# Kernel optimization log

Hardware: AMD Instinct MI355X
Metric: run time of the kernel (lower is better)

The kernel has to match this reference:

```python
import jax, jax.numpy as jnp
import numpy as np

CHANNELS = 1024
PIVOT = 16384


def setup_inputs() -> dict:
    key = jax.random.key(0)
    k1, k2, k3 = jax.random.split(key, 3)
    x_Jx = jax.random.normal(k1, (3 * PIVOT, CHANNELS), dtype=jnp.float32)
    # Linear(channels, channels) params, torch-like init scale
    s = 1.0 / np.sqrt(CHANNELS)
    W = jax.random.uniform(k2, (CHANNELS, CHANNELS), dtype=jnp.float32, minval=-s, maxval=s)
    b = jax.random.uniform(k3, (CHANNELS,), dtype=jnp.float32, minval=-s, maxval=s)
    return {"x_Jx": x_Jx, "W": W, "b": b}


def reference(x_Jx, W, b):
    pivot = x_Jx.shape[0] // 3
    channels = W.shape[0]
    x = x_Jx[:pivot]                                   # [P, C]
    hAx = jnp.tanh(x @ W.T + b)                        # [P, C]
    hpAx = 1.0 - hAx ** 2                              # tanh'
    Jx = x_Jx[pivot:].reshape(pivot, channels, 2)      # [P, C, 2]
    # sum_j W[i,j] * Jx[p,j,k]  (the explicit broadcast-sum in torch is this GEMM)
    WJx = jnp.einsum('ij,pjk->pik', W, Jx)             # [P, C, 2]
    hpAJx = (hpAx[:, :, None] * WJx).reshape(-1, channels)  # [2P, C]
    return jnp.concatenate([hAx, hpAJx], axis=0)       # [3P, C]
```

## Files before the change

### kernel.cpp

```cpp
#include <hip/hip_runtime.h>
#include <hip/hip_bf16.h>
#include <cstdint>

typedef __attribute__((ext_vector_type(8))) short short8;
typedef __attribute__((ext_vector_type(4))) float floatx4;

__device__ __forceinline__ float tanh_fast(float x) {
    float e = __expf(2.0f * x);
    return 1.0f - 2.0f * __builtin_amdgcn_rcpf(e + 1.0f);
}

__device__ __forceinline__ unsigned int bf16_bits(float f) {
    __hip_bfloat16 h = __float2bfloat16(f);
    return (unsigned int)*reinterpret_cast<unsigned short*>(&h);
}
__device__ __forceinline__ unsigned int pack2(float lo, float hi) {
    return bf16_bits(lo) | (bf16_bits(hi) << 16);
}

__device__ __forceinline__ void async16(const void* g, void* l) {
    __builtin_amdgcn_global_load_lds(
        (const __attribute__((address_space(1))) unsigned int*)g,
        (__attribute__((address_space(3))) unsigned int*)l, 16, 0, 0);
}

__device__ __forceinline__ void swizzle_tile(int& row0, int& col0) {
    const int nwg  = gridDim.x * gridDim.y;
    const int flat = blockIdx.y * gridDim.x + blockIdx.x;
    const int swz  = (flat & 7) * (nwg >> 3) + (flat >> 3);
    col0 = (swz & 7) * 128;
    row0 = (swz >> 3) * 128;
}


__global__ __launch_bounds__(256) void cvt_prep(
    const float* __restrict__ X, const float* __restrict__ G,
    const float* __restrict__ W,
    short* __restrict__ Xb, short* __restrict__ Mb, short* __restrict__ Wb,
    int nbX, int nbG)
{
    const int tid = threadIdx.x;
    const int b   = blockIdx.x;
    if (b < nbX) {
        const size_t e = ((size_t)b * 256 + tid) * 16;
        const float4 f0 = *(const float4*)(X + e);
        const float4 f1 = *(const float4*)(X + e + 4);
        const float4 f2 = *(const float4*)(X + e + 8);
        const float4 f3 = *(const float4*)(X + e + 12);
        uint4 o0, o1;
        o0.x = pack2(f0.x, f0.y); o0.y = pack2(f0.z, f0.w);
        o0.z = pack2(f1.x, f1.y); o0.w = pack2(f1.z, f1.w);
        o1.x = pack2(f2.x, f2.y); o1.y = pack2(f2.z, f2.w);
        o1.z = pack2(f3.x, f3.y); o1.w = pack2(f3.z, f3.w);
        *(uint4*)(Xb + e)     = o0;
        *(uint4*)(Xb + e + 8) = o1;
    } else if (b < nbX + nbG) {
        const size_t s = (size_t)(b - nbX) * 256 + tid;
        const size_t p = s >> 7;
        const int    c = (int)(s & 127);
        const float* src = G + p * 2048 + (size_t)c * 16;
        const float4 f0 = *(const float4*)(src);
        const float4 f1 = *(const float4*)(src + 4);
        const float4 f2 = *(const float4*)(src + 8);
        const float4 f3 = *(const float4*)(src + 12);
        uint4 E, O;
        E.x = pack2(f0.x, f0.z); E.y = pack2(f1.x, f1.z);
        E.z = pack2(f2.x, f2.z); E.w = pack2(f3.x, f3.z);
        O.x = pack2(f0.y, f0.w); O.y = pack2(f1.y, f1.w);
        O.z = pack2(f2.y, f2.w); O.w = pack2(f3.y, f3.w);
        *(uint4*)(Mb + (2 * p)     * 1024 + (size_t)c * 8) = E;
        *(uint4*)(Mb + (2 * p + 1) * 1024 + (size_t)c * 8) = O;
    } else {
        const size_t e = ((size_t)(b - nbX - nbG) * 256 + tid) * 16;
        const float4 f0 = *(const float4*)(W + e);
        const float4 f1 = *(const float4*)(W + e + 4);
        const float4 f2 = *(const float4*)(W + e + 8);
        const float4 f3 = *(const float4*)(W + e + 12);
        uint4 o0, o1;
        o0.x = pack2(f0.x, f0.y); o0.y = pack2(f0.z, f0.w);
        o0.z = pack2(f1.x, f1.y); o0.w = pack2(f1.z, f1.w);
        o1.x = pack2(f2.x, f2.y); o1.y = pack2(f2.z, f2.w);
        o1.z = pack2(f3.x, f3.y); o1.w = pack2(f3.z, f3.w);
        *(uint4*)(Wb + e)     = o0;
        *(uint4*)(Wb + e + 8) = o1;
    }
}

#define GEMM_STAGE_AND_MMA(Ag, Bg)                                             \
    for (int k0 = 0; k0 < K; k0 += 64) {                                       \
        __syncthreads();                                                       \
        _Pragma("unroll")                                                      \
        for (int i = 0; i < 4; ++i) {                                          \
            async16(Ag + (size_t)i * 8 * K + k0, Al + i * 512);                \
            async16(Bg + (size_t)i * 8 * K + k0, Bl + i * 512);                \
        }                                                                      \
        __syncthreads();                                                       \
        _Pragma("unroll")                                                      \
        for (int ki = 0; ki < 2; ++ki) {                                       \
            const int kxs = (((ki * 4 + quad) ^ rxor)) * 8;                    \
            short8 af[4], bf[4];                                               \
            _Pragma("unroll")                                                  \
            for (int s = 0; s < 4; ++s)                                        \
                af[s] = *(const short8*)&As[a_base + s * 16 * 64 + kxs];       \
            _Pragma("unroll")                                                  \
            for (int s = 0; s < 4; ++s)                                        \
                bf[s] = *(const short8*)&Bs[b_base + s * 16 * 64 + kxs];       \
            _Pragma("unroll")                                                  \
            for (int a = 0; a < 4; ++a)                                        \
                _Pragma("unroll")                                              \
                for (int b = 0; b < 4; ++b)                                    \
                    acc[a][b] = __builtin_amdgcn_mfma_f32_16x16x32_bf16(       \
                        af[a], bf[b], acc[a][b], 0, 0, 0);                     \
        }                                                                      \
    }

__global__ __launch_bounds__(256) void k1b_gemm_tanh(
    const short* __restrict__ A,
    const short* __restrict__ B,
    const float* __restrict__ Bv,
    float* __restrict__ out, int K)
{
    __shared__ __align__(16) short As[128 * 64];
    __shared__ __align__(16) short Bs[128 * 64];

    const int tid  = threadIdx.x;
    const int lane = tid & 63;
    const int wave = tid >> 6;
    const int wm = wave & 1, wn = wave >> 1;

    int row0, col0;
    swizzle_tile(row0, col0);

    const int l15  = lane & 15;
    const int quad = lane >> 4;
    const int rxor = l15 & 7;
    const int a_base = (wm * 64 + l15) * 64;
    const int b_base = (wn * 64 + l15) * 64;

    const int lrow = lane >> 3;
    const int lcol = lane & 7;
    const int cswz = lcol ^ lrow;
    const short* Ag = A + (size_t)(row0 + wave * 32 + lrow) * K + cswz * 8;
    const short* Bg = B + (size_t)(col0 + wave * 32 + lrow) * K + cswz * 8;
    short* Al = As + wave * 32 * 64;
    short* Bl = Bs + wave * 32 * 64;

    floatx4 acc[4][4];
#pragma unroll
    for (int a = 0; a < 4; ++a)
#pragma unroll
        for (int b = 0; b < 4; ++b) acc[a][b] = (floatx4){0.f, 0.f, 0.f, 0.f};

    GEMM_STAGE_AND_MMA(Ag, Bg)

    float bv[4];
#pragma unroll
    for (int b = 0; b < 4; ++b)
        bv[b] = Bv[col0 + wn * 64 + b * 16 + l15];

#pragma unroll
    for (int a = 0; a < 4; ++a) {
        const int rbase = row0 + wm * 64 + a * 16 + quad * 4;
#pragma unroll
        for (int b = 0; b < 4; ++b) {
            const int n = col0 + wn * 64 + b * 16 + l15;
#pragma unroll
            for (int r = 0; r < 4; ++r)
                out[(size_t)(rbase + r) * 1024 + n] = tanh_fast(acc[a][b][r] + bv[b]);
        }
    }
}

__global__ __launch_bounds__(256) void k2b_gemm_jac(
    const short* __restrict__ A,
    const short* __restrict__ B,
    const float* __restrict__ Hout,
    float* __restrict__ out2, int K)
{
    __shared__ __align__(16) short As[128 * 64];
    __shared__ __align__(16) short Bs[128 * 64];

    const int tid  = threadIdx.x;
    const int lane = tid & 63;
    const int wave = tid >> 6;
    const int wm = wave & 1, wn = wave >> 1;

    int r0, col0;
    swizzle_tile(r0, col0);

    const int l15  = lane & 15;
    const int quad = lane >> 4;
    const int rxor = l15 & 7;
    const int a_base = (wm * 64 + l15) * 64;
    const int b_base = (wn * 64 + l15) * 64;

    const int lrow = lane >> 3;
    const int lcol = lane & 7;
    const int cswz = lcol ^ lrow;
    const short* Ag = A + (size_t)(r0 + wave * 32 + lrow) * K + cswz * 8;
    const short* Bg = B + (size_t)(col0 + wave * 32 + lrow) * K + cswz * 8;
    short* Al = As + wave * 32 * 64;
    short* Bl = Bs + wave * 32 * 64;

    floatx4 acc[4][4];
#pragma unroll
    for (int a = 0; a < 4; ++a)
#pragma unroll
        for (int b = 0; b < 4; ++b) acc[a][b] = (floatx4){0.f, 0.f, 0.f, 0.f};

    GEMM_STAGE_AND_MMA(Ag, Bg)

#pragma unroll
    for (int a = 0; a < 4; ++a) {
        const int rb = r0 + wm * 64 + a * 16 + quad * 4;
#pragma unroll
        for (int b = 0; b < 4; ++b) {
            const int i = col0 + wn * 64 + b * 16 + l15;
            const int shift = (i >= 512) ? 1 : 0;
            const int ccol = 2 * i - shift * 1024;
#pragma unroll
            for (int pr = 0; pr < 2; ++pr) {
                const int re = rb + pr * 2;
                const int p  = re >> 1;
                const float h  = Hout[(size_t)p * 1024 + i];
                const float hp = 1.0f - h * h;
                float2 st;
                st.x = hp * acc[a][b][pr * 2];
                st.y = hp * acc[a][b][pr * 2 + 1];
                *(float2*)&out2[(size_t)(re + shift) * 1024 + ccol] = st;
            }
        }
    }
}

#define LDS_STRIDE 72

__global__ __launch_bounds__(256) void k1_gemm_tanh(
    const float* __restrict__ X, const float* __restrict__ W,
    const float* __restrict__ Bv, float* __restrict__ out, int K)
{
    __shared__ __align__(16) short As[128 * LDS_STRIDE];
    __shared__ __align__(16) short Bs[128 * LDS_STRIDE];
    const int tid  = threadIdx.x;
    const int lane = tid & 63;
    const int wave = tid >> 6;
    const int wm = wave & 1, wn = wave >> 1;
    int row0, col0;
    swizzle_tile(row0, col0);
    const int l15  = lane & 15;
    const int quad = lane >> 4;
    const int a_base = (wm * 64 + l15) * LDS_STRIDE;
    const int b_base = (wn * 64 + l15) * LDS_STRIDE;

    floatx4 acc[4][4];
#pragma unroll
    for (int a = 0; a < 4; ++a)
#pragma unroll
        for (int b = 0; b < 4; ++b) acc[a][b] = (floatx4){0.f, 0.f, 0.f, 0.f};

    for (int k0 = 0; k0 < K; k0 += 64) {
        __syncthreads();
#pragma unroll
        for (int i = 0; i < 8; ++i) {
            const int g = i * 256 + tid;
            const int r = g >> 4, c = g & 15;
            const float4 va = *(const float4*)(X + (size_t)(row0 + r) * K + k0 + c * 4);
            const float4 vb = *(const float4*)(W + (size_t)(col0 + r) * K + k0 + c * 4);
            uint2 ea, eb;
            ea.x = pack2(va.x, va.y); ea.y = pack2(va.z, va.w);
            eb.x = pack2(vb.x, vb.y); eb.y = pack2(vb.z, vb.w);
            *(uint2*)&As[r * LDS_STRIDE + c * 4] = ea;
            *(uint2*)&Bs[r * LDS_STRIDE + c * 4] = eb;
        }
        __syncthreads();
#pragma unroll
        for (int ki = 0; ki < 2; ++ki) {
            const int kx = ki * 32 + quad * 8;
            short8 af[4], bf[4];
#pragma unroll
            for (int s = 0; s < 4; ++s)
                af[s] = *(const short8*)&As[a_base + s * 16 * LDS_STRIDE + kx];
#pragma unroll
            for (int s = 0; s < 4; ++s)
                bf[s] = *(const short8*)&Bs[b_base + s * 16 * LDS_STRIDE + kx];
#pragma unroll
            for (int a = 0; a < 4; ++a)
#pragma unroll
                for (int b = 0; b < 4; ++b)
                    acc[a][b] = __builtin_amdgcn_mfma_f32_16x16x32_bf16(
                        af[a], bf[b], acc[a][b], 0, 0, 0);
        }
    }

    float bv[4];
#pragma unroll
    for (int b = 0; b < 4; ++b)
        bv[b] = Bv[col0 + wn * 64 + b * 16 + l15];
#pragma unroll
    for (int a = 0; a < 4; ++a) {
        const int rbase = row0 + wm * 64 + a * 16 + quad * 4;
#pragma unroll
        for (int b = 0; b < 4; ++b) {
            const int n = col0 + wn * 64 + b * 16 + l15;
#pragma unroll
            for (int r = 0; r < 4; ++r)
                out[(size_t)(rbase + r) * 1024 + n] = tanh_fast(acc[a][b][r] + bv[b]);
        }
    }
}

__global__ __launch_bounds__(256) void k2_gemm_jac(
    const float* __restrict__ G, const float* __restrict__ W,
    const float* __restrict__ Hout, float* __restrict__ out2, int K)
{
    __shared__ __align__(16) short As[128 * LDS_STRIDE];
    __shared__ __align__(16) short Bs[128 * LDS_STRIDE];
    const int tid  = threadIdx.x;
    const int lane = tid & 63;
    const int wave = tid >> 6;
    const int wm = wave & 1, wn = wave >> 1;
    int r0, col0;
    swizzle_tile(r0, col0);
    const int p0 = r0 >> 1;
    const int l15  = lane & 15;
    const int quad = lane >> 4;
    const int a_base = (wm * 64 + l15) * LDS_STRIDE;
    const int b_base = (wn * 64 + l15) * LDS_STRIDE;

    floatx4 acc[4][4];
#pragma unroll
    for (int a = 0; a < 4; ++a)
#pragma unroll
        for (int b = 0; b < 4; ++b) acc[a][b] = (floatx4){0.f, 0.f, 0.f, 0.f};

    for (int k0 = 0; k0 < K; k0 += 64) {
        __syncthreads();
#pragma unroll
        for (int i = 0; i < 8; ++i) {
            const int g = i * 256 + tid;
            const int r = g >> 4, c = g & 15;
            const float4 vb = *(const float4*)(W + (size_t)(col0 + r) * K + k0 + c * 4);
            uint2 eb;
            eb.x = pack2(vb.x, vb.y); eb.y = pack2(vb.z, vb.w);
            *(uint2*)&Bs[r * LDS_STRIDE + c * 4] = eb;
        }
#pragma unroll
        for (int i = 0; i < 4; ++i) {
            const int g = i * 256 + tid;
            const int q = g >> 4, d = g & 15;
            const float* src = G + (size_t)(p0 + q) * 2048 + 2 * k0 + d * 8;
            const float4 u0 = *(const float4*)src;
            const float4 u1 = *(const float4*)(src + 4);
            uint2 E, O;
            E.x = pack2(u0.x, u0.z); E.y = pack2(u1.x, u1.z);
            O.x = pack2(u0.y, u0.w); O.y = pack2(u1.y, u1.w);
            *(uint2*)&As[(2 * q)     * LDS_STRIDE + d * 4] = E;
            *(uint2*)&As[(2 * q + 1) * LDS_STRIDE + d * 4] = O;
        }
        __syncthreads();
#pragma unroll
        for (int ki = 0; ki < 2; ++ki) {
            const int kx = ki * 32 + quad * 8;
            short8 af[4], bf[4];
#pragma unroll
            for (int s = 0; s < 4; ++s)
                af[s] = *(const short8*)&As[a_base + s * 16 * LDS_STRIDE + kx];
#pragma unroll
            for (int s = 0; s < 4; ++s)
                bf[s] = *(const short8*)&Bs[b_base + s * 16 * LDS_STRIDE + kx];
#pragma unroll
            for (int a = 0; a < 4; ++a)
#pragma unroll
                for (int b = 0; b < 4; ++b)
                    acc[a][b] = __builtin_amdgcn_mfma_f32_16x16x32_bf16(
                        af[a], bf[b], acc[a][b], 0, 0, 0);
        }
    }

#pragma unroll
    for (int a = 0; a < 4; ++a) {
        const int rb = r0 + wm * 64 + a * 16 + quad * 4;
#pragma unroll
        for (int b = 0; b < 4; ++b) {
            const int i = col0 + wn * 64 + b * 16 + l15;
            const int shift = (i >= 512) ? 1 : 0;
            const int ccol = 2 * i - shift * 1024;
#pragma unroll
            for (int pr = 0; pr < 2; ++pr) {
                const int re = rb + pr * 2;
                const int p  = re >> 1;
                const float h  = Hout[(size_t)p * 1024 + i];
                const float hp = 1.0f - h * h;
                float2 st;
                st.x = hp * acc[a][b][pr * 2];
                st.y = hp * acc[a][b][pr * 2 + 1];
                *(float2*)&out2[(size_t)(re + shift) * 1024 + ccol] = st;
            }
        }
    }
}

extern "C" void kernel_launch(void* const* d_in, const int* in_sizes, int n_in,
                              void* d_out, int out_size, void* d_ws, size_t ws_size,
                              hipStream_t stream) {
    const float* xJx = (const float*)d_in[0];
    const float* W   = (const float*)d_in[1];
    const float* bv  = (const float*)d_in[2];
    float* out = (float*)d_out;

    const int C     = 1024;
    const int rows3 = in_sizes[0] / C;
    const int pivot = rows3 / 3;

    const size_t szXb = (size_t)pivot * C * 2;
    const size_t szMb = (size_t)2 * pivot * C * 2;
    const size_t szWb = (size_t)C * C * 2;
    dim3 blk(256);

    if (ws_size >= szXb + szMb + szWb) {
        short* Xb = (short*)d_ws;
        short* Mb = (short*)((char*)d_ws + szXb);
        short* Wb = (short*)((char*)d_ws + szXb + szMb);

        const int nbX = (pivot * C) / 4096;
        const int nbG = (pivot * 2 * C) / 4096;
        const int nbW = (C * C) / 4096;
        cvt_prep<<<dim3(nbX + nbG + nbW), blk, 0, stream>>>(
            xJx, xJx + (size_t)pivot * C, W, Xb, Mb, Wb, nbX, nbG);

        dim3 g1(C / 128, pivot / 128);
        k1b_gemm_tanh<<<g1, blk, 0, stream>>>(Xb, Wb, bv, out, C);

        dim3 g2(C / 128, (2 * pivot) / 128);
        k2b_gemm_jac<<<g2, blk, 0, stream>>>(Mb, Wb, out,
                                             out + (size_t)pivot * C, C);
    } else {
        dim3 g1(C / 128, pivot / 128);
        k1_gemm_tanh<<<g1, blk, 0, stream>>>(xJx, W, bv, out, C);
        dim3 g2(C / 128, (2 * pivot) / 128);
        k2_gemm_jac<<<g2, blk, 0, stream>>>(xJx + (size_t)pivot * C, W, out,
                                            out + (size_t)pivot * C, C);
    }
}
```

Measured before the change: 508.5 us.

## Double-buffer LDS tiles to overlap global loads with MFMA compute

Both GEMM kernels (tanh and Jacobian) now use two LDS buffers per operand. The next K-tile's async global-to-LDS loads are issued before the MFMAs on the current tile, which also cuts the loop to one barrier per iteration instead of two. The goal is to hide global memory latency behind matrix math. In exchange LDS per block doubles to 64KB, which can lower the number of resident blocks per CU.

```diff
diff --git a/kernel.cpp b/kernel.cpp
--- a/kernel.cpp
+++ b/kernel.cpp
@@ -86,31 +86,48 @@
     }
 }
 
-#define GEMM_STAGE_AND_MMA(Ag, Bg)                                             \
-    for (int k0 = 0; k0 < K; k0 += 64) {                                       \
-        __syncthreads();                                                       \
+#define GEMM_PIPELINED(Ag, Bg)                                                 \
+    {                                                                          \
+        const int nt = K >> 6;                                                 \
         _Pragma("unroll")                                                      \
         for (int i = 0; i < 4; ++i) {                                          \
-            async16(Ag + (size_t)i * 8 * K + k0, Al + i * 512);                \
-            async16(Bg + (size_t)i * 8 * K + k0, Bl + i * 512);                \
+            async16(Ag + (size_t)i * 8 * K, As + wave * 2048 + i * 512);       \
+            async16(Bg + (size_t)i * 8 * K, Bs + wave * 2048 + i * 512);       \
         }                                                                      \
         __syncthreads();                                                       \
-        _Pragma("unroll")                                                      \
-        for (int ki = 0; ki < 2; ++ki) {                                       \
-            const int kxs = (((ki * 4 + quad) ^ rxor)) * 8;                    \
-            short8 af[4], bf[4];                                               \
+        for (int t = 0; t < nt; ++t) {                                         \
+            const short* Asc = As + (t & 1) * 8192;                            \
+            const short* Bsc = Bs + (t & 1) * 8192;                            \
+            if (t + 1 < nt) {                                                  \
+                short* Asn = As + ((t + 1) & 1) * 8192;                        \
+                short* Bsn = Bs + ((t + 1) & 1) * 8192;                        \
+                const int kn = (t + 1) * 64;                                   \
+                _Pragma("unroll")                                              \
+                for (int i = 0; i < 4; ++i) {                                  \
+                    async16(Ag + (size_t)i * 8 * K + kn,                       \
+                            Asn + wave * 2048 + i * 512);                      \
+                    async16(Bg + (size_t)i * 8 * K + kn,                       \
+                            Bsn + wave * 2048 + i * 512);                      \
+                }                                                              \
+            }                                                                  \
             _Pragma("unroll")                                                  \
-            for (int s = 0; s < 4; ++s)                                        \
-                af[s] = *(const short8*)&As[a_base + s * 16 * 64 + kxs];       \
-            _Pragma("unroll")                                                  \
-            for (int s = 0; s < 4; ++s)                                        \
-                bf[s] = *(const short8*)&Bs[b_base + s * 16 * 64 + kxs];       \
-            _Pragma("unroll")                                                  \
-            for (int a = 0; a < 4; ++a)                                        \
+            for (int ki = 0; ki < 2; ++ki) {                                   \
+                const int kxs = ((ki * 4 + quad) ^ rxor) * 8;                  \
+                short8 af[4], bf[4];                                           \
                 _Pragma("unroll")                                              \
-                for (int b = 0; b < 4; ++b)                                    \
-                    acc[a][b] = __builtin_amdgcn_mfma_f32_16x16x32_bf16(       \
-                        af[a], bf[b], acc[a][b], 0, 0, 0);                     \
+                for (int s = 0; s < 4; ++s)                                    \
+                    af[s] = *(const short8*)&Asc[a_base + s * 1024 + kxs];     \
+                _Pragma("unroll")                                              \
+                for (int s = 0; s < 4; ++s)                                    \
+                    bf[s] = *(const short8*)&Bsc[b_base + s * 1024 + kxs];     \
+                _Pragma("unroll")                                              \
+                for (int a = 0; a < 4; ++a)                                    \
+                    _Pragma("unroll")                                          \
+                    for (int b = 0; b < 4; ++b)                                \
+                        acc[a][b] = __builtin_amdgcn_mfma_f32_16x16x32_bf16(   \
+                            af[a], bf[b], acc[a][b], 0, 0, 0);                 \
+            }                                                                  \
+            __syncthreads();                                                   \
         }                                                                      \
     }
 
@@ -120,8 +137,8 @@
     const float* __restrict__ Bv,
     float* __restrict__ out, int K)
 {
-    __shared__ __align__(16) short As[128 * 64];
-    __shared__ __align__(16) short Bs[128 * 64];
+    __shared__ __align__(16) short As[2 * 128 * 64];
+    __shared__ __align__(16) short Bs[2 * 128 * 64];
 
     const int tid  = threadIdx.x;
     const int lane = tid & 63;
@@ -142,8 +159,6 @@
     const int cswz = lcol ^ lrow;
     const short* Ag = A + (size_t)(row0 + wave * 32 + lrow) * K + cswz * 8;
     const short* Bg = B + (size_t)(col0 + wave * 32 + lrow) * K + cswz * 8;
-    short* Al = As + wave * 32 * 64;
-    short* Bl = Bs + wave * 32 * 64;
 
     floatx4 acc[4][4];
 #pragma unroll
@@ -151,7 +166,7 @@
 #pragma unroll
         for (int b = 0; b < 4; ++b) acc[a][b] = (floatx4){0.f, 0.f, 0.f, 0.f};
 
-    GEMM_STAGE_AND_MMA(Ag, Bg)
+    GEMM_PIPELINED(Ag, Bg)
 
     float bv[4];
 #pragma unroll
@@ -177,8 +192,8 @@
     const float* __restrict__ Hout,
     float* __restrict__ out2, int K)
 {
-    __shared__ __align__(16) short As[128 * 64];
-    __shared__ __align__(16) short Bs[128 * 64];
+    __shared__ __align__(16) short As[2 * 128 * 64];
+    __shared__ __align__(16) short Bs[2 * 128 * 64];
 
     const int tid  = threadIdx.x;
     const int lane = tid & 63;
@@ -199,8 +214,6 @@
     const int cswz = lcol ^ lrow;
     const short* Ag = A + (size_t)(r0 + wave * 32 + lrow) * K + cswz * 8;
     const short* Bg = B + (size_t)(col0 + wave * 32 + lrow) * K + cswz * 8;
-    short* Al = As + wave * 32 * 64;
-    short* Bl = Bs + wave * 32 * 64;
 
     floatx4 acc[4][4];
 #pragma unroll
@@ -208,7 +221,7 @@
 #pragma unroll
         for (int b = 0; b < 4; ++b) acc[a][b] = (floatx4){0.f, 0.f, 0.f, 0.f};
 
-    GEMM_STAGE_AND_MMA(Ag, Bg)
+    GEMM_PIPELINED(Ag, Bg)
 
 #pragma unroll
     for (int a = 0; a < 4; ++a) {
```

Result: no change. 503.5 us (-1.0%).

## Use 256x256 tiles with 8 waves and double-buffered LDS prefetch in bf16 GEMMs

Applied to the files above, without the earlier changes.

The bf16 GEMM kernels move from 128x128 tiles with 4 waves to 256x256 tiles with 8 waves, each wave computing a 128x64 block. The LDS is double-buffered so the next K-slice loads asynchronously while the current one is being multiplied, with one barrier per iteration. MFMA sections are bracketed with s_setprio. The goal is more operand reuse per byte loaded and overlap of global loads with compute. In exchange it uses 128 KB of LDS and 128 accumulator registers per lane, leaving one block per CU, and halves the number of workgroups.

```diff
diff --git a/kernel.cpp b/kernel.cpp
--- a/kernel.cpp
+++ b/kernel.cpp
@@ -24,12 +24,13 @@
         (__attribute__((address_space(3))) unsigned int*)l, 16, 0, 0);
 }
 
-__device__ __forceinline__ void swizzle_tile(int& row0, int& col0) {
-    const int nwg  = gridDim.x * gridDim.y;
-    const int flat = blockIdx.y * gridDim.x + blockIdx.x;
+__device__ __forceinline__ void swizzle_tile_bm(int& row0, int& col0, int bm) {
+    const int gx   = gridDim.x;
+    const int nwg  = gx * gridDim.y;
+    const int flat = blockIdx.y * gx + blockIdx.x;
     const int swz  = (flat & 7) * (nwg >> 3) + (flat >> 3);
-    col0 = (swz & 7) * 128;
-    row0 = (swz >> 3) * 128;
+    col0 = (swz % gx) * bm;
+    row0 = (swz / gx) * bm;
 }
 
 
@@ -86,136 +87,162 @@
     }
 }
 
-#define GEMM_STAGE_AND_MMA(Ag, Bg)                                             \
-    for (int k0 = 0; k0 < K; k0 += 64) {                                       \
-        __syncthreads();                                                       \
+#define STAGE256(dst_d, kt)                                                    \
+    {                                                                          \
+        const int koff = (kt) * 64;                                            \
         _Pragma("unroll")                                                      \
         for (int i = 0; i < 4; ++i) {                                          \
-            async16(Ag + (size_t)i * 8 * K + k0, Al + i * 512);                \
-            async16(Bg + (size_t)i * 8 * K + k0, Bl + i * 512);                \
+            async16(Ag + (size_t)(i * 64) * K + koff,                          \
+                    As + (dst_d) * 16384 + (i * 64 + wave * 8) * 64);          \
+            async16(Bg + (size_t)(i * 64) * K + koff,                          \
+                    Bs + (dst_d) * 16384 + (i * 64 + wave * 8) * 64);          \
         }                                                                      \
-        __syncthreads();                                                       \
-        _Pragma("unroll")                                                      \
-        for (int ki = 0; ki < 2; ++ki) {                                       \
-            const int kxs = (((ki * 4 + quad) ^ rxor)) * 8;                    \
-            short8 af[4], bf[4];                                               \
+    }
+
+#define GEMM256_MAIN()                                                         \
+    {                                                                          \
+        const int NT = K >> 6;                                                 \
+        STAGE256(0, 0)                                                         \
+        asm volatile("s_waitcnt vmcnt(0)" ::: "memory");                       \
+        __builtin_amdgcn_s_barrier();                                          \
+        for (int t = 0; t < NT; ++t) {                                         \
+            const int d = t & 1;                                               \
+            if (t + 1 < NT) STAGE256(d ^ 1, t + 1)                             \
+            const short* Ad = As + d * 16384;                                  \
+            const short* Bd = Bs + d * 16384;                                  \
+            short8 bfr[4][2];                                                  \
             _Pragma("unroll")                                                  \
-            for (int s = 0; s < 4; ++s)                                        \
-                af[s] = *(const short8*)&As[a_base + s * 16 * 64 + kxs];       \
+            for (int n = 0; n < 4; ++n)                                        \
+                _Pragma("unroll")                                              \
+                for (int ki = 0; ki < 2; ++ki)                                 \
+                    bfr[n][ki] = *(const short8*)&Bd[b_base + n * 1024 +       \
+                                     (((ki * 4 + quad) ^ rxor) * 8)];          \
             _Pragma("unroll")                                                  \
-            for (int s = 0; s < 4; ++s)                                        \
-                bf[s] = *(const short8*)&Bs[b_base + s * 16 * 64 + kxs];       \
-            _Pragma("unroll")                                                  \
-            for (int a = 0; a < 4; ++a)                                        \
+            for (int p = 0; p < 4; ++p) {                                      \
+                short8 afr[2][2];                                              \
                 _Pragma("unroll")                                              \
-                for (int b = 0; b < 4; ++b)                                    \
-                    acc[a][b] = __builtin_amdgcn_mfma_f32_16x16x32_bf16(       \
-                        af[a], bf[b], acc[a][b], 0, 0, 0);                     \
+                for (int a2 = 0; a2 < 2; ++a2)                                 \
+                    _Pragma("unroll")                                          \
+                    for (int ki = 0; ki < 2; ++ki)                             \
+                        afr[a2][ki] = *(const short8*)&Ad[a_base +             \
+                            (p * 2 + a2) * 1024 +                              \
+                            (((ki * 4 + quad) ^ rxor) * 8)];                   \
+                __builtin_amdgcn_s_setprio(1);                                 \
+                _Pragma("unroll")                                              \
+                for (int a2 = 0; a2 < 2; ++a2)                                 \
+                    _Pragma("unroll")                                          \
+                    for (int n = 0; n < 4; ++n)                                \
+                        _Pragma("unroll")                                      \
+                        for (int ki = 0; ki < 2; ++ki)                         \
+                            acc[p * 2 + a2][n] =                               \
+                                __builtin_amdgcn_mfma_f32_16x16x32_bf16(       \
+                                    afr[a2][ki], bfr[n][ki],                   \
+                                    acc[p * 2 + a2][n], 0, 0, 0);              \
+                __builtin_amdgcn_s_setprio(0);                                 \
+            }                                                                  \
+            asm volatile("s_waitcnt vmcnt(0)" ::: "memory");                   \
+            __builtin_amdgcn_s_barrier();                                      \
         }                                                                      \
     }
 
-__global__ __launch_bounds__(256) void k1b_gemm_tanh(
+__global__ __launch_bounds__(512, 1) void k1c_gemm_tanh(
     const short* __restrict__ A,
     const short* __restrict__ B,
     const float* __restrict__ Bv,
     float* __restrict__ out, int K)
 {
-    __shared__ __align__(16) short As[128 * 64];
-    __shared__ __align__(16) short Bs[128 * 64];
+    __shared__ __align__(16) short As[2 * 256 * 64];
+    __shared__ __align__(16) short Bs[2 * 256 * 64];
 
     const int tid  = threadIdx.x;
     const int lane = tid & 63;
     const int wave = tid >> 6;
-    const int wm = wave & 1, wn = wave >> 1;
+    const int wr = wave >> 2, wc = wave & 3;
 
     int row0, col0;
-    swizzle_tile(row0, col0);
+    swizzle_tile_bm(row0, col0, 256);
 
     const int l15  = lane & 15;
     const int quad = lane >> 4;
     const int rxor = l15 & 7;
-    const int a_base = (wm * 64 + l15) * 64;
-    const int b_base = (wn * 64 + l15) * 64;
+    const int a_base = (wr * 128 + l15) * 64;
+    const int b_base = (wc * 64  + l15) * 64;
 
     const int lrow = lane >> 3;
     const int lcol = lane & 7;
     const int cswz = lcol ^ lrow;
-    const short* Ag = A + (size_t)(row0 + wave * 32 + lrow) * K + cswz * 8;
-    const short* Bg = B + (size_t)(col0 + wave * 32 + lrow) * K + cswz * 8;
-    short* Al = As + wave * 32 * 64;
-    short* Bl = Bs + wave * 32 * 64;
-
-    floatx4 acc[4][4];
-#pragma unroll
-    for (int a = 0; a < 4; ++a)
-#pragma unroll
-        for (int b = 0; b < 4; ++b) acc[a][b] = (floatx4){0.f, 0.f, 0.f, 0.f};
-
-    GEMM_STAGE_AND_MMA(Ag, Bg)
+    const short* Ag = A + (size_t)(row0 + wave * 8 + lrow) * K + cswz * 8;
+    const short* Bg = B + (size_t)(col0 + wave * 8 + lrow) * K + cswz * 8;
+
+    floatx4 acc[8][4];
+#pragma unroll
+    for (int a = 0; a < 8; ++a)
+#pragma unroll
+        for (int n = 0; n < 4; ++n) acc[a][n] = (floatx4){0.f, 0.f, 0.f, 0.f};
+
+    GEMM256_MAIN()
 
     float bv[4];
 #pragma unroll
-    for (int b = 0; b < 4; ++b)
-        bv[b] = Bv[col0 + wn * 64 + b * 16 + l15];
-
-#pragma unroll
-    for (int a = 0; a < 4; ++a) {
-        const int rbase = row0 + wm * 64 + a * 16 + quad * 4;
-#pragma unroll
-        for (int b = 0; b < 4; ++b) {
-            const int n = col0 + wn * 64 + b * 16 + l15;
+    for (int n = 0; n < 4; ++n)
+        bv[n] = Bv[col0 + wc * 64 + n * 16 + l15];
+
+#pragma unroll
+    for (int a = 0; a < 8; ++a) {
+        const int rbase = row0 + wr * 128 + a * 16 + quad * 4;
+#pragma unroll
+        for (int n = 0; n < 4; ++n) {
+            const int c = col0 + wc * 64 + n * 16 + l15;
 #pragma unroll
             for (int r = 0; r < 4; ++r)
-                out[(size_t)(rbase + r) * 1024 + n] = tanh_fast(acc[a][b][r] + bv[b]);
-        }
-    }
-}
-
-__global__ __launch_bounds__(256) void k2b_gemm_jac(
+                out[(size_t)(rbase + r) * 1024 + c] = tanh_fast(acc[a][n][r] + bv[n]);
+        }
+    }
+}
+
+__global__ __launch_bounds__(512, 1) void k2c_gemm_jac(
     const short* __restrict__ A,
     const short* __restrict__ B,
     const float* __restrict__ Hout,
     float* __restrict__ out2, int K)
 {
-    __shared__ __align__(16) short As[128 * 64];
-    __shared__ __align__(16) short Bs[128 * 64];
+    __shared__ __align__(16) short As[2 * 256 * 64];
+    __shared__ __align__(16) short Bs[2 * 256 * 64];
 
     const int tid  = threadIdx.x;
     const int lane = tid & 63;
     const int wave = tid >> 6;
-    const int wm = wave & 1, wn = wave >> 1;
+    const int wr = wave >> 2, wc = wave & 3;
 
     int r0, col0;
-    swizzle_tile(r0, col0);
+    swizzle_tile_bm(r0, col0, 256);
 
     const int l15  = lane & 15;
     const int quad = lane >> 4;
     const int rxor = l15 & 7;
-    const int a_base = (wm * 64 + l15) * 64;
-    const int b_base = (wn * 64 + l15) * 64;
+    const int a_base = (wr * 128 + l15) * 64;
+    const int b_base = (wc * 64  + l15) * 64;
 
     const int lrow = lane >> 3;
     const int lcol = lane & 7;
     const int cswz = lcol ^ lrow;
-    const short* Ag = A + (size_t)(r0 + wave * 32 + lrow) * K + cswz * 8;
-    const short* Bg = B + (size_t)(col0 + wave * 32 + lrow) * K + cswz * 8;
-    short* Al = As + wave * 32 * 64;
-    short* Bl = Bs + wave * 32 * 64;
-
-    floatx4 acc[4][4];
-#pragma unroll
-    for (int a = 0; a < 4; ++a)
-#pragma unroll
-        for (int b = 0; b < 4; ++b) acc[a][b] = (floatx4){0.f, 0.f, 0.f, 0.f};
-
-    GEMM_STAGE_AND_MMA(Ag, Bg)
-
-#pragma unroll
-    for (int a = 0; a < 4; ++a) {
-        const int rb = r0 + wm * 64 + a * 16 + quad * 4;
-#pragma unroll
-        for (int b = 0; b < 4; ++b) {
-            const int i = col0 + wn * 64 + b * 16 + l15;
+    const short* Ag = A + (size_t)(r0 + wave * 8 + lrow) * K + cswz * 8;
+    const short* Bg = B + (size_t)(col0 + wave * 8 + lrow) * K + cswz * 8;
+
+    floatx4 acc[8][4];
+#pragma unroll
+    for (int a = 0; a < 8; ++a)
+#pragma unroll
+        for (int n = 0; n < 4; ++n) acc[a][n] = (floatx4){0.f, 0.f, 0.f, 0.f};
+
+    GEMM256_MAIN()
+
+#pragma unroll
+    for (int a = 0; a < 8; ++a) {
+        const int rb = r0 + wr * 128 + a * 16 + quad * 4;
+#pragma unroll
+        for (int n = 0; n < 4; ++n) {
+            const int i = col0 + wc * 64 + n * 16 + l15;
             const int shift = (i >= 512) ? 1 : 0;
             const int ccol = 2 * i - shift * 1024;
 #pragma unroll
@@ -225,8 +252,8 @@
                 const float h  = Hout[(size_t)p * 1024 + i];
                 const float hp = 1.0f - h * h;
                 float2 st;
-                st.x = hp * acc[a][b][pr * 2];
-                st.y = hp * acc[a][b][pr * 2 + 1];
+                st.x = hp * acc[a][n][pr * 2];
+                st.y = hp * acc[a][n][pr * 2 + 1];
                 *(float2*)&out2[(size_t)(re + shift) * 1024 + ccol] = st;
             }
         }
@@ -234,6 +261,14 @@
 }
 
 #define LDS_STRIDE 72
+
+__device__ __forceinline__ void swizzle_tile(int& row0, int& col0) {
+    const int nwg  = gridDim.x * gridDim.y;
+    const int flat = blockIdx.y * gridDim.x + blockIdx.x;
+    const int swz  = (flat & 7) * (nwg >> 3) + (flat >> 3);
+    col0 = (swz & 7) * 128;
+    row0 = (swz >> 3) * 128;
+}
 
 __global__ __launch_bounds__(256) void k1_gemm_tanh(
     const float* __restrict__ X, const float* __restrict__ W,
@@ -415,7 +450,6 @@
     const size_t szXb = (size_t)pivot * C * 2;
     const size_t szMb = (size_t)2 * pivot * C * 2;
     const size_t szWb = (size_t)C * C * 2;
-    dim3 blk(256);
 
     if (ws_size >= szXb + szMb + szWb) {
         short* Xb = (short*)d_ws;
@@ -425,20 +459,20 @@
         const int nbX = (pivot * C) / 4096;
         const int nbG = (pivot * 2 * C) / 4096;
         const int nbW = (C * C) / 4096;
-        cvt_prep<<<dim3(nbX + nbG + nbW), blk, 0, stream>>>(
+        cvt_prep<<<dim3(nbX + nbG + nbW), dim3(256), 0, stream>>>(
             xJx, xJx + (size_t)pivot * C, W, Xb, Mb, Wb, nbX, nbG);
 
-        dim3 g1(C / 128, pivot / 128);
-        k1b_gemm_tanh<<<g1, blk, 0, stream>>>(Xb, Wb, bv, out, C);
-
-        dim3 g2(C / 128, (2 * pivot) / 128);
-        k2b_gemm_jac<<<g2, blk, 0, stream>>>(Mb, Wb, out,
-                                             out + (size_t)pivot * C, C);
+        dim3 g1(C / 256, pivot / 256);
+        k1c_gemm_tanh<<<g1, dim3(512), 0, stream>>>(Xb, Wb, bv, out, C);
+
+        dim3 g2(C / 256, (2 * pivot) / 256);
+        k2c_gemm_jac<<<g2, dim3(512), 0, stream>>>(Mb, Wb, out,
+                                                   out + (size_t)pivot * C, C);
     } else {
         dim3 g1(C / 128, pivot / 128);
-        k1_gemm_tanh<<<g1, blk, 0, stream>>>(xJx, W, bv, out, C);
+        k1_gemm_tanh<<<g1, dim3(256), 0, stream>>>(xJx, W, bv, out, C);
         dim3 g2(C / 128, (2 * pivot) / 128);
-        k2_gemm_jac<<<g2, blk, 0, stream>>>(xJx + (size_t)pivot * C, W, out,
-                                            out + (size_t)pivot * C, C);
-    }
-}
+        k2_gemm_jac<<<g2, dim3(256), 0, stream>>>(xJx + (size_t)pivot * C, W, out,
+                                                  out + (size_t)pivot * C, C);
+    }
+}
```

Measured after the change: 483.9 us. 4.8% less time.
